# Optimization experiments

Hardware: AMD Instinct MI355X
Metric: run time of the kernel (lower is better)

The kernel has to match this reference:

```python
import jax, jax.numpy as jnp
import numpy as np

# module hyperparameters (from init_kwargs ch_in=256, ch_out=256, hyper_in=128)
CH_IN, CH_OUT, HYPER_IN = 256, 256, 128
G = max(CH_OUT // 64, 1)            # num_gen = 4
G_IN, G_OUT = CH_IN // G, CH_OUT // G  # 64, 64
NW = G_OUT * G_IN * 9               # 36864 weights per group
NB = G_OUT                          # 64 biases per group
HD = int(max(HYPER_IN, NW + NB) * 0.25 + 0.5 * HYPER_IN) // G  # 2324


def setup_inputs() -> dict:
    key = jax.random.key(0)
    k0, k1, k2, k3 = jax.random.split(key, 4)
    B, H, W = 8, 64, 64
    image = jax.random.normal(k0, (B, CH_IN, H, W), jnp.float32)
    hyper = jax.random.normal(k1, (B, HYPER_IN), jnp.float32)
    # hypernetwork MLP params, stacked over the G generators
    W1 = jax.random.normal(k2, (G, HYPER_IN, HD), jnp.float32) * 0.05
    b1 = jnp.zeros((G, HD), jnp.float32)
    W2 = jax.random.normal(k3, (G, HD, NW + NB), jnp.float32) * 0.01
    b2 = jnp.zeros((G, NW + NB), jnp.float32)
    return {"image": image, "hyper": hyper, "W1": W1, "b1": b1, "W2": W2, "b2": b2}


def _hyperconv(image, hyper, W1, b1, W2, b2):
    B, C, H, W = image.shape
    # per-group hypernetwork: gened[g,b,:] = MLP_g(hyper[b])
    h = jax.nn.relu(jnp.einsum('bi,gid->gbd', hyper, W1) + b1[:, None, :])
    gened = jnp.einsum('gbd,gdo->gbo', h, W2) + b2[:, None, :]  # (G,B,NW+NB)
    w = gened[..., :NW].reshape(G, B, G_OUT, G_IN * 9)
    bias = gened[..., NW:].reshape(G, B, G_OUT)                 # (G,B,G_OUT)
    # 3x3 unfold with padding=1, channel ordering (c, kh, kw) like torch unfold
    xp = jnp.pad(image, ((0, 0), (0, 0), (1, 1), (1, 1)))
    patches = jnp.stack([xp[:, :, i:i + H, j:j + W]
                         for i in range(3) for j in range(3)], axis=2)  # (B,C,9,H,W)
    # block-diagonal weight => grouped dynamic conv: split channels into G groups
    patches = patches.reshape(B, G, G_IN * 9, H * W)
    out = jnp.einsum('gbok,bgkl->bgol', w, patches)             # (B,G,G_OUT,H*W)
    out = out.reshape(B, CH_OUT, H, W)
    bias = jnp.transpose(bias, (1, 0, 2)).reshape(B, CH_OUT, 1, 1)
    return out + bias


def reference(image, hyper, W1, b1, W2, b2):
    return _hyperconv(image, hyper, W1, b1, W2, b2)
```

## Files before the change

kernel.cpp:

```cpp
#include <hip/hip_runtime.h>

#define G 4
#define NBATCH 8
#define HIN 128
#define HD 2324
#define NW 36864
#define NO 36928
#define NO4 (NO / 4)
#define GIN 64
#define GOUT 64
#define HIMG 64
#define WIMG 64
#define CIN 256
#define DSPLIT 8
#define DCHUNK 292

typedef __attribute__((ext_vector_type(8))) short bf16x8;
typedef __attribute__((ext_vector_type(4))) float f32x4;

__device__ inline unsigned short bf16rne(float f) {
  union { float f; unsigned u; } x; x.f = f;
  unsigned r = (x.u + 0x7FFF + ((x.u >> 16) & 1)) >> 16;
  return (unsigned short)r;
}

__global__ __launch_bounds__(256) void k1_hyper_l1(
    const float* __restrict__ hyper, const float* __restrict__ W1,
    const float* __restrict__ b1, float* __restrict__ h_t) {
  int g = blockIdx.y;
  int d = blockIdx.x * 256 + threadIdx.x;
  if (d >= HD) return;
  const float* W1g = W1 + (size_t)g * HIN * HD + d;
  float bias = b1[g * HD + d];
  float acc[NBATCH];
#pragma unroll
  for (int b = 0; b < NBATCH; ++b) acc[b] = bias;
  for (int i = 0; i < HIN; ++i) {
    float wv = W1g[(size_t)i * HD];
#pragma unroll
    for (int b = 0; b < NBATCH; ++b)
      acc[b] = fmaf(hyper[b * HIN + i], wv, acc[b]);
  }
  float4* hp = (float4*)(h_t + ((size_t)g * HD + d) * 8);
  hp[0] = make_float4(fmaxf(acc[0], 0.f), fmaxf(acc[1], 0.f),
                      fmaxf(acc[2], 0.f), fmaxf(acc[3], 0.f));
  hp[1] = make_float4(fmaxf(acc[4], 0.f), fmaxf(acc[5], 0.f),
                      fmaxf(acc[6], 0.f), fmaxf(acc[7], 0.f));
}

#define FMA_D(wv, hoff)                                   \
  {                                                       \
    _Pragma("unroll")                                     \
    for (int b = 0; b < NBATCH; ++b) {                    \
      float hv = hh[(hoff) * 8 + b];                      \
      acc[b][0] = fmaf(hv, (wv)[0], acc[b][0]);           \
      acc[b][1] = fmaf(hv, (wv)[1], acc[b][1]);           \
      acc[b][2] = fmaf(hv, (wv)[2], acc[b][2]);           \
      acc[b][3] = fmaf(hv, (wv)[3], acc[b][3]);           \
    }                                                     \
  }

__global__ __launch_bounds__(256) void k2_hyper_l2(
    const float* __restrict__ h_t, const float* __restrict__ W2,
    float* __restrict__ partial) {
  int g = blockIdx.y, ds = blockIdx.z;
  int o4 = blockIdx.x * 256 + threadIdx.x;
  bool active = (o4 < NO4);
  if (!active) o4 = NO4 - 1;
  const f32x4* W2g = (const f32x4*)(W2 + (size_t)g * HD * NO) + o4;
  const float* hg = h_t + (size_t)g * HD * 8;
  int d0 = ds * DCHUNK;
  int d1 = d0 + DCHUNK; if (d1 > HD) d1 = HD;
  int nd = d1 - d0;

  f32x4 acc[NBATCH] = {};
  const size_t WS = NO4;
  const f32x4* Wp = W2g + (size_t)d0 * WS;
  f32x4 w0 = __builtin_nontemporal_load(Wp);
  f32x4 w1 = __builtin_nontemporal_load(Wp + WS);
  f32x4 w2 = __builtin_nontemporal_load(Wp + 2 * WS);
  f32x4 w3 = __builtin_nontemporal_load(Wp + 3 * WS);
  int dd = 0;
  for (; dd < nd - 4; dd += 4) {
    const f32x4* Wn = Wp + (size_t)(dd + 4) * WS;
    f32x4 n0 = __builtin_nontemporal_load(Wn);
    f32x4 n1 = __builtin_nontemporal_load(Wn + WS);
    f32x4 n2 = __builtin_nontemporal_load(Wn + 2 * WS);
    f32x4 n3 = __builtin_nontemporal_load(Wn + 3 * WS);
    const float* hh = hg + (size_t)(d0 + dd) * 8;
    FMA_D(w0, 0) FMA_D(w1, 1) FMA_D(w2, 2) FMA_D(w3, 3)
    w0 = n0; w1 = n1; w2 = n2; w3 = n3;
  }
  {
    const float* hh = hg + (size_t)(d0 + dd) * 8;
    FMA_D(w0, 0) FMA_D(w1, 1) FMA_D(w2, 2) FMA_D(w3, 3)
  }

  if (active) {
    f32x4* pout = (f32x4*)partial + ((size_t)ds * G * NBATCH + g * NBATCH) * NO4 + o4;
#pragma unroll
    for (int b = 0; b < NBATCH; ++b) pout[(size_t)b * NO4] = acc[b];
  }
}

__global__ __launch_bounds__(256) void k_wprep(
    const float* __restrict__ partial, const float* __restrict__ b2,
    short* __restrict__ wbf, float* __restrict__ bias_f) {
  int gb = blockIdx.y;
  int g = gb >> 3;
  if (blockIdx.x == 144) {
    int o = threadIdx.x;
    if (o < GOUT) {
      float s = b2[(size_t)g * NO + NW + o];
#pragma unroll
      for (int ds = 0; ds < DSPLIT; ++ds)
        s += partial[((size_t)ds * G * NBATCH + gb) * NO + NW + o];
      bias_f[gb * GOUT + o] = s;
    }
    return;
  }
  int q = blockIdx.x * 256 + threadIdx.x;
  int c = q & 63, rest = q >> 6;
  int o = rest & 63, k = rest >> 6;
  int f = o * 576 + c * 9 + k;
  float s = b2[(size_t)g * NO + f];
#pragma unroll
  for (int ds = 0; ds < DSPLIT; ++ds)
    s += partial[((size_t)ds * G * NBATCH + gb) * NO + f];
  wbf[(size_t)gb * 9 * 4096 + q] = (short)bf16rne(s);
}

__global__ __launch_bounds__(256) void k_iprep(
    const float* __restrict__ image, short* __restrict__ imgt) {
  int row = blockIdx.x;
  int g = blockIdx.y, b = blockIdx.z;
  int gb = g * NBATCH + b;
  int tid = threadIdx.x;
  short* rowp = imgt + ((size_t)gb * 66 + row) * 66 * 64;
  if (row == 0 || row == 65) {
    uint4 z = {0, 0, 0, 0};
    uint4* p = (uint4*)rowp;
#pragma unroll
    for (int i = 0; i < 3; ++i) {
      int idx = tid + i * 256;
      if (idx < 528) p[idx] = z;
    }
    return;
  }
  int y = row - 1;
  __shared__ float lds[64 * 65];
  int p = tid & 63, cg = tid >> 6;
#pragma unroll
  for (int i = 0; i < 16; ++i) {
    int c = cg * 16 + i;
    lds[p * 65 + c] = image[((size_t)b * CIN + g * GIN + c) * 4096 + y * 64 + p];
  }
  __syncthreads();
  int p2 = tid >> 2, cq = tid & 3;
  unsigned short tmp[16];
#pragma unroll
  for (int i = 0; i < 16; ++i) tmp[i] = bf16rne(lds[p2 * 65 + cq * 16 + i]);
  short* dst = rowp + (p2 + 1) * 64 + cq * 16;
  *(uint4*)dst = *(uint4*)&tmp[0];
  *(uint4*)(dst + 8) = *(uint4*)&tmp[8];
  if (tid < 16) {
    ((uint2*)rowp)[tid] = make_uint2(0, 0);
  } else if (tid < 32) {
    ((uint2*)(rowp + 65 * 64))[tid - 16] = make_uint2(0, 0);
  }
}

__global__ __launch_bounds__(256) void k3_mfma(
    const short* __restrict__ wbf, const short* __restrict__ imgt,
    const float* __restrict__ bias_f, float* __restrict__ outbuf) {
  int g = blockIdx.y, b = blockIdx.z;
  int gb = g * NBATCH + b;
  int ygrp = blockIdx.x & 15;
  int tid = threadIdx.x;
  int w = tid >> 6, l = tid & 63;
  int y = ygrp * 4 + w;
  int lo = l & 15;
  int hi = l >> 4;

  const short* wgb = wbf + (size_t)gb * 9 * 4096;
  const short* ibase = imgt + (((size_t)gb * 66 + y) * 66 + lo) * 64 + hi * 8;

  f32x4 acc[4][4] = {};
  bf16x8 a0[4], b0[4], a1[4], b1[4];

#define LA(dst, ks) { int s_ = (ks) >> 1, h_ = (ks) & 1;                      \
    const short* p_ = wgb + (size_t)s_ * 4096 + lo * 64 + h_ * 32 + hi * 8;   \
    _Pragma("unroll") for (int m_ = 0; m_ < 4; ++m_)                          \
      dst[m_] = *(const bf16x8*)(p_ + m_ * 1024); }
#define LB(dst, ks) { int s_ = (ks) >> 1, h_ = (ks) & 1;                      \
    int dy_ = s_ / 3, dx_ = s_ - 3 * dy_;                                     \
    const short* p_ = ibase + ((size_t)dy_ * 66 + dx_) * 64 + h_ * 32;        \
    _Pragma("unroll") for (int n_ = 0; n_ < 4; ++n_)                          \
      dst[n_] = *(const bf16x8*)(p_ + n_ * 1024); }
#define MM(aa, bb) { _Pragma("unroll") for (int m_ = 0; m_ < 4; ++m_)         \
    _Pragma("unroll") for (int n_ = 0; n_ < 4; ++n_)                          \
      acc[m_][n_] = __builtin_amdgcn_mfma_f32_16x16x32_bf16(                  \
          aa[m_], bb[n_], acc[m_][n_], 0, 0, 0); }

  LA(a0, 0) LB(b0, 0)
#pragma unroll
  for (int it = 0; it < 9; ++it) {
    LA(a1, 2 * it + 1) LB(b1, 2 * it + 1)
    MM(a0, b0)
    if (it < 8) { LA(a0, 2 * it + 2) LB(b0, 2 * it + 2) }
    MM(a1, b1)
  }

  float* op = outbuf + ((size_t)b * CIN + g * GOUT) * 4096 + y * 64;
#pragma unroll
  for (int m = 0; m < 4; ++m)
#pragma unroll
    for (int j = 0; j < 4; ++j) {
      int o = m * 16 + hi * 4 + j;
      float bias = bias_f[gb * 64 + o];
#pragma unroll
      for (int n = 0; n < 4; ++n)
        op[(size_t)o * 4096 + n * 16 + lo] = acc[m][n][j] + bias;
    }
#undef LA
#undef LB
#undef MM
}

extern "C" void kernel_launch(void* const* d_in, const int* in_sizes, int n_in,
                              void* d_out, int out_size, void* d_ws, size_t ws_size,
                              hipStream_t stream) {
  const float* image = (const float*)d_in[0];
  const float* hyper = (const float*)d_in[1];
  const float* W1    = (const float*)d_in[2];
  const float* b1    = (const float*)d_in[3];
  const float* W2    = (const float*)d_in[4];
  const float* b2    = (const float*)d_in[5];
  float* out = (float*)d_out;

  float* h_t     = (float*)d_ws;
  float* bias_f  = h_t + (size_t)G * HD * 8;
  float* partial = bias_f + G * NBATCH * GOUT;
  short* wbf     = (short*)(partial + (size_t)DSPLIT * G * NBATCH * NO);
  short* imgt    = wbf + (size_t)G * NBATCH * 9 * 4096;

  k_iprep<<<dim3(66, G, NBATCH), 256, 0, stream>>>(image, imgt);
  k1_hyper_l1<<<dim3((HD + 255) / 256, G), 256, 0, stream>>>(hyper, W1, b1, h_t);
  k2_hyper_l2<<<dim3((NO4 + 255) / 256, G, DSPLIT), 256, 0, stream>>>(h_t, W2, partial);
  k_wprep<<<dim3(145, G * NBATCH), 256, 0, stream>>>(partial, b2, wbf, bias_f);
  k3_mfma<<<dim3(16, G, NBATCH), 256, 0, stream>>>(wbf, imgt, bias_f, out);
}
```

Baseline: 313.7 us.

## Coalesce weight-prep reads via LDS transpose and split conv output channels across blocks

k_wprep now reads the partial sums and b2 as contiguous float4 vectors, reduces them, scatters the bf16 results into shared memory in the (k, o, c) layout, then writes them out coalesced. This replaces the previous strided gather, where each thread read one scalar at a 9-element stride. The launch shrinks from 145 blocks per group-batch to 5 (4 weight blocks of 16 output rows plus 1 bias block). Separately, the MFMA conv kernel splits its 64 output channels into two halves across blocks, doubling the grid to 1024 blocks and halving accumulator registers, at the cost of loading the image tiles twice.

Result: slower. 323.4 us (+3.1%).

```diff
diff --git a/kernel.cpp b/kernel.cpp
--- a/kernel.cpp
+++ b/kernel.cpp
@@ -108,26 +108,48 @@
     short* __restrict__ wbf, float* __restrict__ bias_f) {
   int gb = blockIdx.y;
   int g = gb >> 3;
-  if (blockIdx.x == 144) {
-    int o = threadIdx.x;
-    if (o < GOUT) {
-      float s = b2[(size_t)g * NO + NW + o];
+  int tid = threadIdx.x;
+  if (blockIdx.x == 4) {
+    if (tid < GOUT) {
+      float s = b2[(size_t)g * NO + NW + tid];
 #pragma unroll
       for (int ds = 0; ds < DSPLIT; ++ds)
-        s += partial[((size_t)ds * G * NBATCH + gb) * NO + NW + o];
-      bias_f[gb * GOUT + o] = s;
+        s += partial[((size_t)ds * G * NBATCH + gb) * NO + NW + tid];
+      bias_f[gb * GOUT + tid] = s;
     }
     return;
   }
-  int q = blockIdx.x * 256 + threadIdx.x;
-  int c = q & 63, rest = q >> 6;
-  int o = rest & 63, k = rest >> 6;
-  int f = o * 576 + c * 9 + k;
-  float s = b2[(size_t)g * NO + f];
-#pragma unroll
-  for (int ds = 0; ds < DSPLIT; ++ds)
-    s += partial[((size_t)ds * G * NBATCH + gb) * NO + f];
-  wbf[(size_t)gb * 9 * 4096 + q] = (short)bf16rne(s);
+  __shared__ short lds[9216];
+  int o0 = blockIdx.x * 16;
+  const f32x4* b2p = (const f32x4*)(b2 + (size_t)g * NO) + o0 * 144;
+  const f32x4* pbase = (const f32x4*)partial + (size_t)gb * NO4 + o0 * 144;
+#pragma unroll
+  for (int j = 0; j < 9; ++j) {
+    int idx4 = tid + j * 256;
+    f32x4 s = b2p[idx4];
+#pragma unroll
+    for (int ds = 0; ds < DSPLIT; ++ds) {
+      f32x4 v = pbase[(size_t)ds * G * NBATCH * NO4 + idx4];
+      s[0] += v[0]; s[1] += v[1]; s[2] += v[2]; s[3] += v[3];
+    }
+    int flbase = idx4 * 4;
+#pragma unroll
+    for (int e = 0; e < 4; ++e) {
+      int fl = flbase + e;
+      int ol = fl / 576;
+      int rest = fl - ol * 576;
+      int c = rest / 9, k = rest - c * 9;
+      lds[k * 1024 + ol * 64 + c] = (short)bf16rne(s[e]);
+    }
+  }
+  __syncthreads();
+  short* wout = wbf + (size_t)gb * NW;
+#pragma unroll
+  for (int j = 0; j < 9; ++j) {
+    int u = tid + j * 256;
+    int k = u >> 8, rem = u & 255;
+    ((uint2*)(wout + (size_t)k * 4096 + o0 * 64))[rem] = ((uint2*)lds)[u];
+  }
 }
 
 __global__ __launch_bounds__(256) void k_iprep(
@@ -175,29 +197,29 @@
     const float* __restrict__ bias_f, float* __restrict__ outbuf) {
   int g = blockIdx.y, b = blockIdx.z;
   int gb = g * NBATCH + b;
-  int ygrp = blockIdx.x & 15;
+  int ygrp = blockIdx.x >> 1, ms = blockIdx.x & 1;
   int tid = threadIdx.x;
   int w = tid >> 6, l = tid & 63;
   int y = ygrp * 4 + w;
   int lo = l & 15;
   int hi = l >> 4;
 
-  const short* wgb = wbf + (size_t)gb * 9 * 4096;
+  const short* wgb = wbf + (size_t)gb * 9 * 4096 + (size_t)ms * 32 * 64;
   const short* ibase = imgt + (((size_t)gb * 66 + y) * 66 + lo) * 64 + hi * 8;
 
-  f32x4 acc[4][4] = {};
-  bf16x8 a0[4], b0[4], a1[4], b1[4];
+  f32x4 acc[2][4] = {};
+  bf16x8 a0[2], b0[4], a1[2], b1[4];
 
 #define LA(dst, ks) { int s_ = (ks) >> 1, h_ = (ks) & 1;                      \
     const short* p_ = wgb + (size_t)s_ * 4096 + lo * 64 + h_ * 32 + hi * 8;   \
-    _Pragma("unroll") for (int m_ = 0; m_ < 4; ++m_)                          \
+    _Pragma("unroll") for (int m_ = 0; m_ < 2; ++m_)                          \
       dst[m_] = *(const bf16x8*)(p_ + m_ * 1024); }
 #define LB(dst, ks) { int s_ = (ks) >> 1, h_ = (ks) & 1;                      \
     int dy_ = s_ / 3, dx_ = s_ - 3 * dy_;                                     \
     const short* p_ = ibase + ((size_t)dy_ * 66 + dx_) * 64 + h_ * 32;        \
     _Pragma("unroll") for (int n_ = 0; n_ < 4; ++n_)                          \
       dst[n_] = *(const bf16x8*)(p_ + n_ * 1024); }
-#define MM(aa, bb) { _Pragma("unroll") for (int m_ = 0; m_ < 4; ++m_)         \
+#define MM(aa, bb) { _Pragma("unroll") for (int m_ = 0; m_ < 2; ++m_)         \
     _Pragma("unroll") for (int n_ = 0; n_ < 4; ++n_)                          \
       acc[m_][n_] = __builtin_amdgcn_mfma_f32_16x16x32_bf16(                  \
           aa[m_], bb[n_], acc[m_][n_], 0, 0, 0); }
@@ -213,10 +235,10 @@
 
   float* op = outbuf + ((size_t)b * CIN + g * GOUT) * 4096 + y * 64;
 #pragma unroll
-  for (int m = 0; m < 4; ++m)
+  for (int m = 0; m < 2; ++m)
 #pragma unroll
     for (int j = 0; j < 4; ++j) {
-      int o = m * 16 + hi * 4 + j;
+      int o = ms * 32 + m * 16 + hi * 4 + j;
       float bias = bias_f[gb * 64 + o];
 #pragma unroll
       for (int n = 0; n < 4; ++n)
@@ -247,6 +269,6 @@
   k_iprep<<<dim3(66, G, NBATCH), 256, 0, stream>>>(image, imgt);
   k1_hyper_l1<<<dim3((HD + 255) / 256, G), 256, 0, stream>>>(hyper, W1, b1, h_t);
   k2_hyper_l2<<<dim3((NO4 + 255) / 256, G, DSPLIT), 256, 0, stream>>>(h_t, W2, partial);
-  k_wprep<<<dim3(145, G * NBATCH), 256, 0, stream>>>(partial, b2, wbf, bias_f);
-  k3_mfma<<<dim3(16, G, NBATCH), 256, 0, stream>>>(wbf, imgt, bias_f, out);
-}
+  k_wprep<<<dim3(5, G * NBATCH), 256, 0, stream>>>(partial, b2, wbf, bias_f);
+  k3_mfma<<<dim3(32, G, NBATCH), 256, 0, stream>>>(wbf, imgt, bias_f, out);
+}
```
